# Kernel tuning notes

Measured on AMD Instinct MI355X. Metric: run time of the kernel, lower is better.

Reference implementation:

```python
import jax, jax.numpy as jnp
import numpy as np

VOCAB = 50257
NUM_TAGS = 50
EMB_DIM = 128
CTX = 2
N_TOKENS = 262144


def setup_inputs() -> dict:
    key = jax.random.key(0)
    k1, k2, k3, k4 = jax.random.split(key, 4)
    tokens = jax.random.randint(k1, (N_TOKENS,), 0, VOCAB, dtype=jnp.int64 if jax.config.jax_enable_x64 else jnp.int32)
    emb_table = jax.random.normal(k2, (VOCAB, EMB_DIM), dtype=jnp.float32)
    W = jax.random.normal(k3, (NUM_TAGS, EMB_DIM * (1 + 2 * CTX)), dtype=jnp.float32) * 0.05
    b = jax.random.normal(k4, (NUM_TAGS,), dtype=jnp.float32) * 0.05
    return {"tokens": tokens, "emb_table": emb_table, "W": W, "b": b}


def reference(tokens, emb_table, W, b):
    # [N, D] embedding gather
    emb = emb_table[tokens]
    n = emb.shape[0]
    # zero-pad CTX positions on each side (matches torch.zeros_like padding)
    padded = jnp.pad(emb, ((CTX, CTX), (0, 0)))
    # sliding window concat: [N, (2*CTX+1)*D] via 2*CTX+1 shifted views
    windows = jnp.concatenate([padded[i:i + n] for i in range(2 * CTX + 1)], axis=-1)
    logits = windows @ W.T + b  # [N, num_tags]
    log_probs = jax.nn.log_softmax(logits, axis=-1)
    return log_probs
```

## Files before the change

### kernel.cpp

```cpp
#include <hip/hip_runtime.h>
#include <hip/hip_bf16.h>

#define VOCAB 50257
#define NTAGS 50
#define EMB   128
#define NTOK  262144
#define KD    640
#define WPAD  64

#define TPB   64
#define TOKPB 64
#define ROWS  68
#define STEPS 20

typedef __attribute__((ext_vector_type(4))) float f32x4;
typedef __attribute__((ext_vector_type(8))) short bf16x8;

__device__ __forceinline__ ushort f2bf(float f) {
    union { float f; unsigned u; } v; v.f = f;
    unsigned u = v.u;
    return (ushort)((u + 0x7fffu + ((u >> 16) & 1u)) >> 16);
}

__device__ __forceinline__ void gload_lds16(const void* g, void* l) {
    __builtin_amdgcn_global_load_lds(
        (const __attribute__((address_space(1))) unsigned*)g,
        (__attribute__((address_space(3))) unsigned*)l, 16, 0, 0);
}

__global__ void conv_k(const float* __restrict__ emb, const float* __restrict__ W,
                       ushort* __restrict__ embb, ushort* __restrict__ wb) {
    const int etotal = (VOCAB + 1) * EMB;
    int idx = (blockIdx.x * blockDim.x + threadIdx.x) * 4;
    if (idx < etotal) {
        float4 v = {0.f, 0.f, 0.f, 0.f};
        if (idx < VOCAB * EMB) v = *(const float4*)(emb + idx);
        ushort4 o = { f2bf(v.x), f2bf(v.y), f2bf(v.z), f2bf(v.w) };
        *(ushort4*)(embb + idx) = o;
    } else {
        int wi = idx - etotal;
        if (wi < WPAD * KD) {
            #pragma unroll
            for (int k = 0; k < 4; ++k) {
                int j = wi + k;
                int tag = j / KD;
                wb[j] = f2bf(tag < NTAGS ? W[j] : 0.f);
            }
        }
    }
}

__global__ __launch_bounds__(TPB, 2)
void tagger_k(const int* __restrict__ tokens, const ushort* __restrict__ embb,
              const ushort* __restrict__ Wb, const float* __restrict__ bias,
              float* __restrict__ out) {
    __shared__ ushort smem[ROWS * EMB];

    const int lane = threadIdx.x & 63;
    const int c = lane & 15;
    const int q = lane >> 4;
    const int bb = blockIdx.x * TOKPB;
    const int rsub = lane >> 4;

    int tokid[17];
    #pragma unroll
    for (int g = 0; g < 17; ++g) {
        int t = bb - 2 + g * 4 + rsub;
        tokid[g] = (t >= 0 && t < NTOK) ? tokens[t] : VOCAB;
    }

    const ushort* bp[4];
    #pragma unroll
    for (int nt = 0; nt < 4; ++nt)
        bp[nt] = Wb + (nt * 16 + c) * KD + q * 8;

    bf16x8 Bb[4][4];
    #pragma unroll
    for (int s = 0; s < 4; ++s)
        #pragma unroll
        for (int nt = 0; nt < 4; ++nt)
            Bb[s][nt] = *(const bf16x8*)(bp[nt] + (s >> 2) * 128 + (s & 3) * 32);

    float bv[4];
    #pragma unroll
    for (int nt = 0; nt < 4; ++nt) {
        int tag = nt * 16 + c;
        bv[nt] = bias[tag < NTAGS ? tag : NTAGS - 1];
    }

    {
        const int pc = lane & 15;
        #pragma unroll
        for (int g = 0; g < 17; ++g) {
            int i = g * 4 + rsub;
            int sc = pc ^ (i & 7);
            gload_lds16(embb + (size_t)tokid[g] * EMB + sc * 8, (char*)smem + g * 1024);
        }
    }
    __syncthreads();

    f32x4 acc[4][4];
    #pragma unroll
    for (int mt = 0; mt < 4; ++mt)
        #pragma unroll
        for (int nt = 0; nt < 4; ++nt)
            acc[mt][nt] = (f32x4){0.f, 0.f, 0.f, 0.f};

    bf16x8 Ab[2][4];
    #pragma unroll
    for (int s = 0; s < 2; ++s) {
        int p = s >> 2, kk = s & 3;
        int h = (c + p) & 7;
        int ch = (4 * kk + q) ^ h;
        const char* ab = (const char*)smem + (c + p) * 256 + ch * 16;
        #pragma unroll
        for (int mt = 0; mt < 4; ++mt)
            Ab[s][mt] = *(const bf16x8*)(ab + mt * 4096);
    }

    #pragma unroll
    for (int s = 0; s < STEPS; ++s) {
        __builtin_amdgcn_s_setprio(1);
        #pragma unroll
        for (int mt = 0; mt < 4; ++mt)
            #pragma unroll
            for (int nt = 0; nt < 4; ++nt)
                acc[mt][nt] = __builtin_amdgcn_mfma_f32_16x16x32_bf16(
                    Ab[s & 1][mt], Bb[s & 3][nt], acc[mt][nt], 0, 0, 0);
        __builtin_amdgcn_s_setprio(0);
        if (s + 4 < STEPS) {
            const int t = s + 4, p = t >> 2, kk = t & 3;
            #pragma unroll
            for (int nt = 0; nt < 4; ++nt)
                Bb[s & 3][nt] = *(const bf16x8*)(bp[nt] + p * 128 + kk * 32);
        }
        if (s + 2 < STEPS) {
            const int t = s + 2, p = t >> 2, kk = t & 3;
            int h = (c + p) & 7;
            int ch = (4 * kk + q) ^ h;
            const char* ab = (const char*)smem + (c + p) * 256 + ch * 16;
            #pragma unroll
            for (int mt = 0; mt < 4; ++mt)
                Ab[s & 1][mt] = *(const bf16x8*)(ab + mt * 4096);
        }
    }

    #pragma unroll
    for (int mt = 0; mt < 4; ++mt) {
        #pragma unroll
        for (int j = 0; j < 4; ++j) {
            const int row = bb + mt * 16 + q * 4 + j;
            float v[4];
            float m = -1e30f;
            #pragma unroll
            for (int nt = 0; nt < 4; ++nt) {
                float x = acc[mt][nt][j] + bv[nt];
                v[nt] = x;
                if (nt * 16 + c < NTAGS) m = fmaxf(m, x);
            }
            #pragma unroll
            for (int mask = 8; mask >= 1; mask >>= 1)
                m = fmaxf(m, __shfl_xor(m, mask));
            float s = 0.f;
            #pragma unroll
            for (int nt = 0; nt < 4; ++nt)
                if (nt * 16 + c < NTAGS) s += __expf(v[nt] - m);
            #pragma unroll
            for (int mask = 8; mask >= 1; mask >>= 1)
                s += __shfl_xor(s, mask);
            const float L = m + __logf(s);
            #pragma unroll
            for (int nt = 0; nt < 4; ++nt) {
                int tag = nt * 16 + c;
                if (tag < NTAGS) out[row * NTAGS + tag] = v[nt] - L;
            }
        }
    }
}

extern "C" void kernel_launch(void* const* d_in, const int* in_sizes, int n_in,
                              void* d_out, int out_size, void* d_ws, size_t ws_size,
                              hipStream_t stream) {
    const int*   tokens = (const int*)d_in[0];
    const float* emb    = (const float*)d_in[1];
    const float* W      = (const float*)d_in[2];
    const float* b      = (const float*)d_in[3];
    float* out = (float*)d_out;

    ushort* embb = (ushort*)d_ws;
    ushort* Wb   = embb + (size_t)(VOCAB + 1) * EMB;

    {
        const int etotal = (VOCAB + 1) * EMB;
        const int total4 = (etotal + WPAD * KD) / 4;
        conv_k<<<(total4 + 255) / 256, 256, 0, stream>>>(emb, W, embb, Wb);
    }
    {
        const int nblk = NTOK / TOKPB;
        tagger_k<<<nblk, TPB, 0, stream>>>(tokens, embb, Wb, b, out);
    }
}
```

Baseline: 74.19 us.

## Swap MFMA operand roles so tags map to rows and tokens to columns

Transposes the per-wave GEMM so the weight tile becomes the A operand (tags along rows) and the embeddings become the B operand, with four overlapping token groups (offsets 0,16,32,44) covering 60 tokens per block. Each lane now holds contiguous tags for one token, so log-softmax reduces across only two cross-lane shuffles and outputs are written as float4/float2 vector stores instead of scalar stores. A padded bias buffer is produced in the conversion kernel for vector loads. The trade is redundant compute on overlapping tokens (64 columns for 60 tokens), more blocks, and a partial final block.

```diff
diff --git a/kernel.cpp b/kernel.cpp
--- a/kernel.cpp
+++ b/kernel.cpp
@@ -9,8 +9,8 @@
 #define WPAD  64
 
 #define TPB   64
-#define TOKPB 64
-#define ROWS  68
+#define TOKPB 60
+#define ROWS  64
 #define STEPS 20
 
 typedef __attribute__((ext_vector_type(4))) float f32x4;
@@ -29,7 +29,9 @@
 }
 
 __global__ void conv_k(const float* __restrict__ emb, const float* __restrict__ W,
-                       ushort* __restrict__ embb, ushort* __restrict__ wb) {
+                       const float* __restrict__ b,
+                       ushort* __restrict__ embb, ushort* __restrict__ wb,
+                       float* __restrict__ biasp) {
     const int etotal = (VOCAB + 1) * EMB;
     int idx = (blockIdx.x * blockDim.x + threadIdx.x) * 4;
     if (idx < etotal) {
@@ -37,14 +39,21 @@
         if (idx < VOCAB * EMB) v = *(const float4*)(emb + idx);
         ushort4 o = { f2bf(v.x), f2bf(v.y), f2bf(v.z), f2bf(v.w) };
         *(ushort4*)(embb + idx) = o;
+    } else if (idx < etotal + WPAD * KD) {
+        int wi = idx - etotal;
+        #pragma unroll
+        for (int k = 0; k < 4; ++k) {
+            int j = wi + k;
+            int tag = j / KD;
+            wb[j] = f2bf(tag < NTAGS ? W[j] : 0.f);
+        }
     } else {
-        int wi = idx - etotal;
-        if (wi < WPAD * KD) {
+        int wi = idx - etotal - WPAD * KD;
+        if (wi < WPAD) {
             #pragma unroll
             for (int k = 0; k < 4; ++k) {
                 int j = wi + k;
-                int tag = j / KD;
-                wb[j] = f2bf(tag < NTAGS ? W[j] : 0.f);
+                biasp[j] = (j < NTAGS) ? b[j] : 0.f;
             }
         }
     }
@@ -52,7 +61,7 @@
 
 __global__ __launch_bounds__(TPB, 2)
 void tagger_k(const int* __restrict__ tokens, const ushort* __restrict__ embb,
-              const ushort* __restrict__ Wb, const float* __restrict__ bias,
+              const ushort* __restrict__ Wb, const float* __restrict__ biasp,
               float* __restrict__ out) {
     __shared__ ushort smem[ROWS * EMB];
 
@@ -60,38 +69,40 @@
     const int c = lane & 15;
     const int q = lane >> 4;
     const int bb = blockIdx.x * TOKPB;
-    const int rsub = lane >> 4;
-
-    int tokid[17];
-    #pragma unroll
-    for (int g = 0; g < 17; ++g) {
+    const int rsub = q;
+
+    const int O[4] = {0, 16, 32, 44};
+
+    int tokid[16];
+    #pragma unroll
+    for (int g = 0; g < 16; ++g) {
         int t = bb - 2 + g * 4 + rsub;
         tokid[g] = (t >= 0 && t < NTOK) ? tokens[t] : VOCAB;
     }
 
     const ushort* bp[4];
     #pragma unroll
-    for (int nt = 0; nt < 4; ++nt)
-        bp[nt] = Wb + (nt * 16 + c) * KD + q * 8;
-
-    bf16x8 Bb[4][4];
+    for (int mt = 0; mt < 4; ++mt)
+        bp[mt] = Wb + (mt * 16 + c) * KD + q * 8;
+
+    bf16x8 Wr[4][4];
     #pragma unroll
     for (int s = 0; s < 4; ++s)
         #pragma unroll
-        for (int nt = 0; nt < 4; ++nt)
-            Bb[s][nt] = *(const bf16x8*)(bp[nt] + (s >> 2) * 128 + (s & 3) * 32);
-
-    float bv[4];
-    #pragma unroll
-    for (int nt = 0; nt < 4; ++nt) {
-        int tag = nt * 16 + c;
-        bv[nt] = bias[tag < NTAGS ? tag : NTAGS - 1];
+        for (int mt = 0; mt < 4; ++mt)
+            Wr[s][mt] = *(const bf16x8*)(bp[mt] + (s >> 2) * 128 + (s & 3) * 32);
+
+    float bvv[4][4];
+    #pragma unroll
+    for (int mt = 0; mt < 4; ++mt) {
+        float4 t4 = *(const float4*)(biasp + mt * 16 + q * 4);
+        bvv[mt][0] = t4.x; bvv[mt][1] = t4.y; bvv[mt][2] = t4.z; bvv[mt][3] = t4.w;
     }
 
     {
-        const int pc = lane & 15;
-        #pragma unroll
-        for (int g = 0; g < 17; ++g) {
+        const int pc = c;
+        #pragma unroll
+        for (int g = 0; g < 16; ++g) {
             int i = g * 4 + rsub;
             int sc = pc ^ (i & 7);
             gload_lds16(embb + (size_t)tokid[g] * EMB + sc * 8, (char*)smem + g * 1024);
@@ -106,16 +117,16 @@
         for (int nt = 0; nt < 4; ++nt)
             acc[mt][nt] = (f32x4){0.f, 0.f, 0.f, 0.f};
 
-    bf16x8 Ab[2][4];
+    bf16x8 Er[2][4];
     #pragma unroll
     for (int s = 0; s < 2; ++s) {
         int p = s >> 2, kk = s & 3;
-        int h = (c + p) & 7;
-        int ch = (4 * kk + q) ^ h;
-        const char* ab = (const char*)smem + (c + p) * 256 + ch * 16;
-        #pragma unroll
-        for (int mt = 0; mt < 4; ++mt)
-            Ab[s][mt] = *(const bf16x8*)(ab + mt * 4096);
+        #pragma unroll
+        for (int nt = 0; nt < 4; ++nt) {
+            int r  = O[nt] + c + p;
+            int ch = (4 * kk + q) ^ (r & 7);
+            Er[s][nt] = *(const bf16x8*)((const char*)smem + r * 256 + ch * 16);
+        }
     }
 
     #pragma unroll
@@ -126,53 +137,60 @@
             #pragma unroll
             for (int nt = 0; nt < 4; ++nt)
                 acc[mt][nt] = __builtin_amdgcn_mfma_f32_16x16x32_bf16(
-                    Ab[s & 1][mt], Bb[s & 3][nt], acc[mt][nt], 0, 0, 0);
+                    Wr[s & 3][mt], Er[s & 1][nt], acc[mt][nt], 0, 0, 0);
         __builtin_amdgcn_s_setprio(0);
         if (s + 4 < STEPS) {
             const int t = s + 4, p = t >> 2, kk = t & 3;
             #pragma unroll
-            for (int nt = 0; nt < 4; ++nt)
-                Bb[s & 3][nt] = *(const bf16x8*)(bp[nt] + p * 128 + kk * 32);
+            for (int mt = 0; mt < 4; ++mt)
+                Wr[s & 3][mt] = *(const bf16x8*)(bp[mt] + p * 128 + kk * 32);
         }
         if (s + 2 < STEPS) {
             const int t = s + 2, p = t >> 2, kk = t & 3;
-            int h = (c + p) & 7;
-            int ch = (4 * kk + q) ^ h;
-            const char* ab = (const char*)smem + (c + p) * 256 + ch * 16;
-            #pragma unroll
-            for (int mt = 0; mt < 4; ++mt)
-                Ab[s & 1][mt] = *(const bf16x8*)(ab + mt * 4096);
-        }
-    }
-
-    #pragma unroll
-    for (int mt = 0; mt < 4; ++mt) {
-        #pragma unroll
-        for (int j = 0; j < 4; ++j) {
-            const int row = bb + mt * 16 + q * 4 + j;
-            float v[4];
-            float m = -1e30f;
             #pragma unroll
             for (int nt = 0; nt < 4; ++nt) {
-                float x = acc[mt][nt][j] + bv[nt];
-                v[nt] = x;
-                if (nt * 16 + c < NTAGS) m = fmaxf(m, x);
-            }
-            #pragma unroll
-            for (int mask = 8; mask >= 1; mask >>= 1)
-                m = fmaxf(m, __shfl_xor(m, mask));
-            float s = 0.f;
-            #pragma unroll
-            for (int nt = 0; nt < 4; ++nt)
-                if (nt * 16 + c < NTAGS) s += __expf(v[nt] - m);
-            #pragma unroll
-            for (int mask = 8; mask >= 1; mask >>= 1)
-                s += __shfl_xor(s, mask);
-            const float L = m + __logf(s);
-            #pragma unroll
-            for (int nt = 0; nt < 4; ++nt) {
-                int tag = nt * 16 + c;
-                if (tag < NTAGS) out[row * NTAGS + tag] = v[nt] - L;
+                int r  = O[nt] + c + p;
+                int ch = (4 * kk + q) ^ (r & 7);
+                Er[s & 1][nt] = *(const bf16x8*)((const char*)smem + r * 256 + ch * 16);
+            }
+        }
+    }
+
+    #pragma unroll
+    for (int nt = 0; nt < 4; ++nt) {
+        const int token = bb + O[nt] + c;
+        float x[4][4];
+        float m = -1e30f;
+        #pragma unroll
+        for (int mt = 0; mt < 4; ++mt)
+            #pragma unroll
+            for (int j = 0; j < 4; ++j) {
+                float v = acc[mt][nt][j] + bvv[mt][j];
+                if (mt == 3 && !(q == 0 && j < 2)) v = -1e30f;
+                x[mt][j] = v;
+                m = fmaxf(m, v);
+            }
+        m = fmaxf(m, __shfl_xor(m, 16));
+        m = fmaxf(m, __shfl_xor(m, 32));
+        float ssum = 0.f;
+        #pragma unroll
+        for (int mt = 0; mt < 4; ++mt)
+            #pragma unroll
+            for (int j = 0; j < 4; ++j)
+                ssum += __expf(x[mt][j] - m);
+        ssum += __shfl_xor(ssum, 16);
+        ssum += __shfl_xor(ssum, 32);
+        const float L = m + __logf(ssum);
+        if (token < NTOK) {
+            float* op = out + (size_t)token * NTAGS;
+            #pragma unroll
+            for (int mt = 0; mt < 3; ++mt) {
+                float4 st = { x[mt][0] - L, x[mt][1] - L, x[mt][2] - L, x[mt][3] - L };
+                *(float4*)(op + mt * 16 + q * 4) = st;
+            }
+            if (q == 0) {
+                float2 st2 = { x[3][0] - L, x[3][1] - L };
+                *(float2*)(op + 48) = st2;
             }
         }
     }
@@ -187,16 +205,17 @@
     const float* b      = (const float*)d_in[3];
     float* out = (float*)d_out;
 
-    ushort* embb = (ushort*)d_ws;
-    ushort* Wb   = embb + (size_t)(VOCAB + 1) * EMB;
+    ushort* embb  = (ushort*)d_ws;
+    ushort* Wb    = embb + (size_t)(VOCAB + 1) * EMB;
+    float*  biasp = (float*)(Wb + (size_t)WPAD * KD);
 
     {
         const int etotal = (VOCAB + 1) * EMB;
-        const int total4 = (etotal + WPAD * KD) / 4;
-        conv_k<<<(total4 + 255) / 256, 256, 0, stream>>>(emb, W, embb, Wb);
+        const int total4 = (etotal + WPAD * KD + WPAD) / 4;
+        conv_k<<<(total4 + 255) / 256, 256, 0, stream>>>(emb, W, b, embb, Wb, biasp);
     }
     {
-        const int nblk = NTOK / TOKPB;
-        tagger_k<<<nblk, TPB, 0, stream>>>(tokens, embb, Wb, b, out);
-    }
-}
+        const int nblk = (NTOK + TOKPB - 1) / TOKPB;
+        tagger_k<<<nblk, TPB, 0, stream>>>(tokens, embb, Wb, biasp, out);
+    }
+}
```

Result: slower. 77.19 us (+4.0%).

## Precompute per-vocab projected logits table and gather-sum windows per token

Applied to the files above, without the earlier changes.

Multiplies the embedding table by each of the five window slices of W once per vocabulary entry, producing a bf16 table ZT of shape vocab×320. The tagger then gathers five 64-wide rows per token, sums them with the bias, and applies log-softmax per thread. This replaces the per-token 640-deep GEMM over gathered embeddings with a vocab-sized GEMM (about 5x fewer rows than tokens) and a cheap gather-add. The cost is an extra intermediate written and read in bf16, which adds rounding on the logits, plus a fallback path when the workspace is too small.

```diff
diff --git a/kernel.cpp b/kernel.cpp
--- a/kernel.cpp
+++ b/kernel.cpp
@@ -8,10 +8,9 @@
 #define KD    640
 #define WPAD  64
 
-#define TPB   64
-#define TOKPB 64
-#define ROWS  68
-#define STEPS 20
+#define TAGP  64
+#define NZ    320
+#define ZROWS 50304
 
 typedef __attribute__((ext_vector_type(4))) float f32x4;
 typedef __attribute__((ext_vector_type(8))) short bf16x8;
@@ -28,8 +27,148 @@
         (__attribute__((address_space(3))) unsigned*)l, 16, 0, 0);
 }
 
-__global__ void conv_k(const float* __restrict__ emb, const float* __restrict__ W,
-                       ushort* __restrict__ embb, ushort* __restrict__ wb) {
+__global__ void conv2_k(const float* __restrict__ W, const float* __restrict__ b,
+                        ushort* __restrict__ Wt, float* __restrict__ biasp) {
+    int i = blockIdx.x * blockDim.x + threadIdx.x;
+    if (i < NZ * EMB / 4) {
+        int j = i * 4;
+        int n = j / EMB, d = j % EMB;
+        int p = n >> 6, tg = n & 63;
+        ushort4 o = {0, 0, 0, 0};
+        if (tg < NTAGS) {
+            float4 w4 = *(const float4*)(W + tg * KD + p * EMB + d);
+            o = { f2bf(w4.x), f2bf(w4.y), f2bf(w4.z), f2bf(w4.w) };
+        }
+        *(ushort4*)(Wt + j) = o;
+    } else {
+        int k = i - NZ * EMB / 4;
+        if (k < TAGP / 4) {
+            #pragma unroll
+            for (int e = 0; e < 4; ++e) {
+                int j = k * 4 + e;
+                biasp[j] = (j < NTAGS) ? b[j] : 0.f;
+            }
+        }
+    }
+}
+
+__global__ __launch_bounds__(64)
+void zt_k(const float* __restrict__ emb, const ushort* __restrict__ Wt,
+          ushort* __restrict__ ZT) {
+    const int lane = threadIdx.x & 63;
+    const int c = lane & 15, q = lane >> 4;
+    const int vb = blockIdx.x * 64;
+
+    bf16x8 A[4][4];
+    #pragma unroll
+    for (int mt = 0; mt < 4; ++mt) {
+        int row = vb + mt * 16 + c;
+        bool ok = row < VOCAB;
+        const float* rp = emb + (size_t)(ok ? row : 0) * EMB;
+        #pragma unroll
+        for (int kk = 0; kk < 4; ++kk) {
+            float4 lo = {0,0,0,0}, hi = {0,0,0,0};
+            if (ok) {
+                lo = *(const float4*)(rp + kk * 32 + q * 8);
+                hi = *(const float4*)(rp + kk * 32 + q * 8 + 4);
+            }
+            bf16x8 a;
+            a[0]=(short)f2bf(lo.x); a[1]=(short)f2bf(lo.y);
+            a[2]=(short)f2bf(lo.z); a[3]=(short)f2bf(lo.w);
+            a[4]=(short)f2bf(hi.x); a[5]=(short)f2bf(hi.y);
+            a[6]=(short)f2bf(hi.z); a[7]=(short)f2bf(hi.w);
+            A[mt][kk] = a;
+        }
+    }
+
+    #pragma unroll
+    for (int ng = 0; ng < 5; ++ng) {
+        bf16x8 B[4][4];
+        #pragma unroll
+        for (int nt = 0; nt < 4; ++nt)
+            #pragma unroll
+            for (int kk = 0; kk < 4; ++kk)
+                B[nt][kk] = *(const bf16x8*)(Wt + (ng * 64 + nt * 16 + c) * EMB
+                                                + kk * 32 + q * 8);
+        f32x4 acc[4][4];
+        #pragma unroll
+        for (int mt = 0; mt < 4; ++mt)
+            #pragma unroll
+            for (int nt = 0; nt < 4; ++nt)
+                acc[mt][nt] = (f32x4){0.f, 0.f, 0.f, 0.f};
+        #pragma unroll
+        for (int kk = 0; kk < 4; ++kk)
+            #pragma unroll
+            for (int mt = 0; mt < 4; ++mt)
+                #pragma unroll
+                for (int nt = 0; nt < 4; ++nt)
+                    acc[mt][nt] = __builtin_amdgcn_mfma_f32_16x16x32_bf16(
+                        A[mt][kk], B[nt][kk], acc[mt][nt], 0, 0, 0);
+        #pragma unroll
+        for (int mt = 0; mt < 4; ++mt)
+            #pragma unroll
+            for (int j = 0; j < 4; ++j) {
+                int row = vb + mt * 16 + q * 4 + j;
+                #pragma unroll
+                for (int nt = 0; nt < 4; ++nt)
+                    ZT[(size_t)row * NZ + ng * 64 + nt * 16 + c] =
+                        f2bf(acc[mt][nt][j]);
+            }
+    }
+}
+
+__global__ __launch_bounds__(256)
+void tag_k(const int* __restrict__ tokens, const ushort* __restrict__ ZT,
+           const float* __restrict__ biasp, float* __restrict__ out) {
+    const int t = blockIdx.x * 256 + threadIdx.x;
+    int v[5];
+    #pragma unroll
+    for (int p = 0; p < 5; ++p) {
+        int tt = t + p - 2;
+        v[p] = (tt >= 0 && tt < NTOK) ? tokens[tt] : VOCAB;
+    }
+    float acc[56];
+    #pragma unroll
+    for (int g = 0; g < 14; ++g) {
+        float4 b4 = *(const float4*)(biasp + g * 4);
+        acc[g*4+0] = b4.x; acc[g*4+1] = b4.y; acc[g*4+2] = b4.z; acc[g*4+3] = b4.w;
+    }
+
+    bf16x8 b0[7], b1[7];
+#define ISSUE(P, BUF) { const ushort* rp_ = ZT + (size_t)v[P] * NZ + (P) * TAGP;  \
+        _Pragma("unroll") for (int i_ = 0; i_ < 7; ++i_)                           \
+            BUF[i_] = *(const bf16x8*)(rp_ + i_ * 8); }
+#define CONSUME(BUF) { _Pragma("unroll") for (int i_ = 0; i_ < 7; ++i_)            \
+        { _Pragma("unroll") for (int e_ = 0; e_ < 8; ++e_) {                       \
+            unsigned u_ = (unsigned)(ushort)BUF[i_][e_] << 16;                     \
+            acc[i_*8+e_] += __uint_as_float(u_); } } }
+
+    ISSUE(0, b0) ISSUE(1, b1)
+    CONSUME(b0)  ISSUE(2, b0)
+    CONSUME(b1)  ISSUE(3, b1)
+    CONSUME(b0)  ISSUE(4, b0)
+    CONSUME(b1)
+    CONSUME(b0)
+#undef ISSUE
+#undef CONSUME
+
+    float m = acc[0];
+    #pragma unroll
+    for (int j = 1; j < NTAGS; ++j) m = fmaxf(m, acc[j]);
+    float s = 0.f;
+    #pragma unroll
+    for (int j = 0; j < NTAGS; ++j) s += __expf(acc[j] - m);
+    const float L = m + __logf(s);
+    float* op = out + (size_t)t * NTAGS;
+    #pragma unroll
+    for (int g = 0; g < 25; ++g) {
+        float2 st = { acc[g*2] - L, acc[g*2+1] - L };
+        *(float2*)(op + g * 2) = st;
+    }
+}
+
+__global__ void fb_conv_k(const float* __restrict__ emb, const float* __restrict__ W,
+                          ushort* __restrict__ embb, ushort* __restrict__ wb) {
     const int etotal = (VOCAB + 1) * EMB;
     int idx = (blockIdx.x * blockDim.x + threadIdx.x) * 4;
     if (idx < etotal) {
@@ -50,16 +189,15 @@
     }
 }
 
-__global__ __launch_bounds__(TPB, 2)
-void tagger_k(const int* __restrict__ tokens, const ushort* __restrict__ embb,
+__global__ __launch_bounds__(64, 2)
+void fb_tag_k(const int* __restrict__ tokens, const ushort* __restrict__ embb,
               const ushort* __restrict__ Wb, const float* __restrict__ bias,
               float* __restrict__ out) {
-    __shared__ ushort smem[ROWS * EMB];
-
+    __shared__ ushort smem[68 * EMB];
     const int lane = threadIdx.x & 63;
     const int c = lane & 15;
     const int q = lane >> 4;
-    const int bb = blockIdx.x * TOKPB;
+    const int bb = blockIdx.x * 64;
     const int rsub = lane >> 4;
 
     int tokid[17];
@@ -68,26 +206,22 @@
         int t = bb - 2 + g * 4 + rsub;
         tokid[g] = (t >= 0 && t < NTOK) ? tokens[t] : VOCAB;
     }
-
     const ushort* bp[4];
     #pragma unroll
     for (int nt = 0; nt < 4; ++nt)
         bp[nt] = Wb + (nt * 16 + c) * KD + q * 8;
-
     bf16x8 Bb[4][4];
     #pragma unroll
     for (int s = 0; s < 4; ++s)
         #pragma unroll
         for (int nt = 0; nt < 4; ++nt)
             Bb[s][nt] = *(const bf16x8*)(bp[nt] + (s >> 2) * 128 + (s & 3) * 32);
-
     float bv[4];
     #pragma unroll
     for (int nt = 0; nt < 4; ++nt) {
         int tag = nt * 16 + c;
         bv[nt] = bias[tag < NTAGS ? tag : NTAGS - 1];
     }
-
     {
         const int pc = lane & 15;
         #pragma unroll
@@ -105,21 +239,18 @@
         #pragma unroll
         for (int nt = 0; nt < 4; ++nt)
             acc[mt][nt] = (f32x4){0.f, 0.f, 0.f, 0.f};
-
     bf16x8 Ab[2][4];
     #pragma unroll
     for (int s = 0; s < 2; ++s) {
         int p = s >> 2, kk = s & 3;
-        int h = (c + p) & 7;
-        int ch = (4 * kk + q) ^ h;
+        int ch = (4 * kk + q) ^ ((c + p) & 7);
         const char* ab = (const char*)smem + (c + p) * 256 + ch * 16;
         #pragma unroll
         for (int mt = 0; mt < 4; ++mt)
             Ab[s][mt] = *(const bf16x8*)(ab + mt * 4096);
     }
-
-    #pragma unroll
-    for (int s = 0; s < STEPS; ++s) {
+    #pragma unroll
+    for (int s = 0; s < 20; ++s) {
         __builtin_amdgcn_s_setprio(1);
         #pragma unroll
         for (int mt = 0; mt < 4; ++mt)
@@ -128,35 +259,33 @@
                 acc[mt][nt] = __builtin_amdgcn_mfma_f32_16x16x32_bf16(
                     Ab[s & 1][mt], Bb[s & 3][nt], acc[mt][nt], 0, 0, 0);
         __builtin_amdgcn_s_setprio(0);
-        if (s + 4 < STEPS) {
-            const int t = s + 4, p = t >> 2, kk = t & 3;
+        if (s + 4 < 20) {
+            const int tt = s + 4, p = tt >> 2, kk = tt & 3;
             #pragma unroll
             for (int nt = 0; nt < 4; ++nt)
                 Bb[s & 3][nt] = *(const bf16x8*)(bp[nt] + p * 128 + kk * 32);
         }
-        if (s + 2 < STEPS) {
-            const int t = s + 2, p = t >> 2, kk = t & 3;
-            int h = (c + p) & 7;
-            int ch = (4 * kk + q) ^ h;
+        if (s + 2 < 20) {
+            const int tt = s + 2, p = tt >> 2, kk = tt & 3;
+            int ch = (4 * kk + q) ^ ((c + p) & 7);
             const char* ab = (const char*)smem + (c + p) * 256 + ch * 16;
             #pragma unroll
             for (int mt = 0; mt < 4; ++mt)
                 Ab[s & 1][mt] = *(const bf16x8*)(ab + mt * 4096);
         }
     }
-
     #pragma unroll
     for (int mt = 0; mt < 4; ++mt) {
         #pragma unroll
         for (int j = 0; j < 4; ++j) {
             const int row = bb + mt * 16 + q * 4 + j;
-            float v[4];
+            float x[4];
             float m = -1e30f;
             #pragma unroll
             for (int nt = 0; nt < 4; ++nt) {
-                float x = acc[mt][nt][j] + bv[nt];
-                v[nt] = x;
-                if (nt * 16 + c < NTAGS) m = fmaxf(m, x);
+                float xv = acc[mt][nt][j] + bv[nt];
+                x[nt] = xv;
+                if (nt * 16 + c < NTAGS) m = fmaxf(m, xv);
             }
             #pragma unroll
             for (int mask = 8; mask >= 1; mask >>= 1)
@@ -164,7 +293,7 @@
             float s = 0.f;
             #pragma unroll
             for (int nt = 0; nt < 4; ++nt)
-                if (nt * 16 + c < NTAGS) s += __expf(v[nt] - m);
+                if (nt * 16 + c < NTAGS) s += __expf(x[nt] - m);
             #pragma unroll
             for (int mask = 8; mask >= 1; mask >>= 1)
                 s += __shfl_xor(s, mask);
@@ -172,7 +301,7 @@
             #pragma unroll
             for (int nt = 0; nt < 4; ++nt) {
                 int tag = nt * 16 + c;
-                if (tag < NTAGS) out[row * NTAGS + tag] = v[nt] - L;
+                if (tag < NTAGS) out[row * NTAGS + tag] = x[nt] - L;
             }
         }
     }
@@ -187,16 +316,20 @@
     const float* b      = (const float*)d_in[3];
     float* out = (float*)d_out;
 
-    ushort* embb = (ushort*)d_ws;
-    ushort* Wb   = embb + (size_t)(VOCAB + 1) * EMB;
-
-    {
+    const size_t NEED = 82432ull + (size_t)ZROWS * NZ * 2ull;
+    if (ws_size >= NEED) {
+        ushort* Wt    = (ushort*)d_ws;
+        float*  biasp = (float*)((char*)d_ws + 81920);
+        ushort* ZT    = (ushort*)((char*)d_ws + 82432);
+        conv2_k<<<41, 256, 0, stream>>>(W, b, Wt, biasp);
+        zt_k<<<ZROWS / 64, 64, 0, stream>>>(emb, Wt, ZT);
+        tag_k<<<NTOK / 256, 256, 0, stream>>>(tokens, ZT, biasp, out);
+    } else {
+        ushort* embb = (ushort*)d_ws;
+        ushort* Wb   = embb + (size_t)(VOCAB + 1) * EMB;
         const int etotal = (VOCAB + 1) * EMB;
         const int total4 = (etotal + WPAD * KD) / 4;
-        conv_k<<<(total4 + 255) / 256, 256, 0, stream>>>(emb, W, embb, Wb);
-    }
-    {
-        const int nblk = NTOK / TOKPB;
-        tagger_k<<<nblk, TPB, 0, stream>>>(tokens, embb, Wb, b, out);
-    }
-}
+        fb_conv_k<<<(total4 + 255) / 256, 256, 0, stream>>>(emb, W, embb, Wb);
+        fb_tag_k<<<NTOK / 64, 64, 0, stream>>>(tokens, embb, Wb, b, out);
+    }
+}
```

New measurement: 86.38 us. +16.4%, slower.
